# Optimization experiments

Hardware: AMD Instinct MI355X
Metric: run time of the kernel (lower is better)

## Reference

```python
import jax, jax.numpy as jnp
import numpy as np


def _diag_perm(h, w):
    # Matches torch loop: offsets -(h-1)..w-1, within offset ordered by row i.
    ii, jj = np.meshgrid(np.arange(h), np.arange(w), indexing='ij')
    idx = np.lexsort((ii.ravel(), (jj - ii).ravel())).astype(np.int32)
    inv = np.argsort(idx).astype(np.int32)
    return jnp.asarray(idx), jnp.asarray(inv)


def _mamba(tok, ln_g, ln_b, Win, conv_w, conv_b, Wx, Wdt, bdt, A_log, Dp, Wout):
    # tok: (B, L, C). MambaLayer = LayerNorm + standard Mamba block.
    di, dc = conv_w.shape
    ds = A_log.shape[-1]
    dtr = Wdt.shape[-1]
    mu = tok.mean(-1, keepdims=True)
    var = ((tok - mu) ** 2).mean(-1, keepdims=True)
    t = (tok - mu) * jax.lax.rsqrt(var + 1e-5) * ln_g + ln_b
    xz = jnp.einsum('blc,ec->ble', t, Win)          # (B,L,2*di)
    xh, z = jnp.split(xz, 2, axis=-1)
    # causal depthwise conv over sequence
    xc = jnp.transpose(xh, (0, 2, 1))               # (B,di,L)
    xc = jax.lax.conv_general_dilated(
        xc, conv_w[:, None, :], (1,), [(dc - 1, 0)],
        dimension_numbers=('NCH', 'OIH', 'NCH'), feature_group_count=di)
    u = jax.nn.silu(jnp.transpose(xc, (0, 2, 1)) + conv_b)  # (B,L,di)
    proj = jnp.einsum('bld,ed->ble', u, Wx)
    dt_r, Bm, Cm = jnp.split(proj, [dtr, dtr + ds], axis=-1)
    dt = jax.nn.softplus(jnp.einsum('blr,dr->bld', dt_r, Wdt) + bdt)  # (B,L,di)
    A = -jnp.exp(A_log)                              # (di,ds)

    def step(h, inp):
        dt_t, B_t, C_t, u_t = inp                    # (B,di) (B,ds) (B,ds) (B,di)
        dA = jnp.exp(dt_t[..., None] * A)            # (B,di,ds)
        h = dA * h + dt_t[..., None] * B_t[:, None, :] * u_t[..., None]
        y = jnp.einsum('bds,bs->bd', h, C_t)
        return h, y

    h0 = jnp.zeros((u.shape[0], di, ds), u.dtype)
    _, ys = jax.lax.scan(step, h0, (jnp.moveaxis(dt, 1, 0), jnp.moveaxis(Bm, 1, 0),
                                    jnp.moveaxis(Cm, 1, 0), jnp.moveaxis(u, 1, 0)))
    y = jnp.moveaxis(ys, 0, 1) + u * Dp              # (B,L,di)
    y = y * jax.nn.silu(z)
    return jnp.einsum('bld,cd->blc', y, Wout)


def _forward(x, ln_g, ln_b, Win, conv_w, conv_b, Wx, Wdt, bdt, A_log, Dp, Wout):
    b, c, h, w = x.shape
    idx, inv = _diag_perm(h, w)

    def mam(d, tok):
        return _mamba(tok, ln_g[d], ln_b[d], Win[d], conv_w[d], conv_b[d],
                      Wx[d], Wdt[d], bdt[d], A_log[d], Dp[d], Wout[d])

    row_tok = x.reshape(b, c, h * w).transpose(0, 2, 1)
    row_feat = mam(0, row_tok).transpose(0, 2, 1).reshape(b, c, h, w)
    col_tok = x.transpose(0, 1, 3, 2).reshape(b, c, w * h).transpose(0, 2, 1)
    col_feat = mam(1, col_tok).transpose(0, 2, 1).reshape(b, c, w, h).transpose(0, 1, 3, 2)
    diag_feat = mam(2, row_tok[:, idx, :])[:, inv, :].transpose(0, 2, 1).reshape(b, c, h, w)
    xf = x[:, :, :, ::-1]
    anti_tok = xf.reshape(b, c, h * w).transpose(0, 2, 1)[:, idx, :]
    anti_feat = mam(3, anti_tok)[:, inv, :].transpose(0, 2, 1).reshape(b, c, h, w)[:, :, :, ::-1]
    gate = jax.nn.sigmoid((row_feat + col_feat + diag_feat + anti_feat) / 4.0)
    return x * gate


def setup_inputs() -> dict:
    key = jax.random.key(0)
    ks = jax.random.split(key, 8)
    B, C, H, W = 4, 96, 48, 48
    DI, DS, DC, DTR = 192, 16, 4, 6
    s = 0.05
    return {
        'x': jax.random.normal(ks[0], (B, C, H, W), jnp.float32),
        'ln_g': jnp.ones((4, C), jnp.float32),
        'ln_b': jnp.zeros((4, C), jnp.float32),
        'Win': jax.random.normal(ks[1], (4, 2 * DI, C), jnp.float32) * s,
        'conv_w': jax.random.normal(ks[2], (4, DI, DC), jnp.float32) * s,
        'conv_b': jnp.zeros((4, DI), jnp.float32),
        'Wx': jax.random.normal(ks[3], (4, DTR + 2 * DS, DI), jnp.float32) * s,
        'Wdt': jax.random.normal(ks[4], (4, DI, DTR), jnp.float32) * s,
        'bdt': jax.random.normal(ks[5], (4, DI), jnp.float32) * s,
        'A_log': jnp.log(jnp.broadcast_to(jnp.arange(1, DS + 1, dtype=jnp.float32), (4, DI, DS))),
        'Dp': jnp.ones((4, DI), jnp.float32),
        'Wout': jax.random.normal(ks[6], (4, C, DI), jnp.float32) * s,
    }


def reference(x, ln_g, ln_b, Win, conv_w, conv_b, Wx, Wdt, bdt, A_log, Dp, Wout):
    return _forward(x, ln_g, ln_b, Win, conv_w, conv_b, Wx, Wdt, bdt, A_log, Dp, Wout)
```

## Files before the change

### kernel.cpp

```cpp
#include <hip/hip_runtime.h>
#include <math.h>

#define LSEQ 2304
#define LC 32
#define NCH 72

typedef unsigned short u16;
typedef unsigned int u32;
typedef __attribute__((ext_vector_type(8))) short bf16x8;
typedef __attribute__((ext_vector_type(4))) float f32x4;

__device__ __forceinline__ float sigmoidf_(float v){ return 1.f/(1.f+__expf(-v)); }
__device__ __forceinline__ u16 f2b(float f){
  union{float f; u32 u;} v; v.f = f;
  u32 r = v.u + 0x7fffu + ((v.u >> 16) & 1u);
  return (u16)(r >> 16);
}
__device__ __forceinline__ float b2f(u16 h){
  union{u32 u; float f;} v; v.u = ((u32)h) << 16; return v.f;
}
__device__ __forceinline__ u16 f2h(float f){
  _Float16 h = (_Float16)f;
  union{_Float16 h; u16 u;} v; v.h = h; return v.u;
}
__device__ __forceinline__ float h2f(u16 u){
  union{u16 u; _Float16 h;} v; v.u = u; return (float)v.h;
}
__device__ __forceinline__ uint2 pack4(float a, float b, float c, float d){
  uint2 o;
  o.x = (u32)f2b(a) | ((u32)f2b(b) << 16);
  o.y = (u32)f2b(c) | ((u32)f2b(d) << 16);
  return o;
}
__device__ __forceinline__ float softplus_(float v){
  return fmaxf(v, 0.f) + __logf(1.f + __expf(-fabsf(v)));
}

__global__ void g_kernel(int* __restrict__ g, int* __restrict__ flag){
  int tid = threadIdx.x;
  if (tid == 0) *flag = 1;
  for (int l = tid; l < LSEQ; l += 256){
    g[l] = l;
    g[LSEQ + l] = (l % 48) * 48 + l / 48;
  }
  for (int p = tid; p < LSEQ; p += 256){
    int i = p / 48, j = p % 48, dd = j - i;
    int off = (dd <= 0) ? (47 + dd) * (48 + dd) / 2
                        : 1176 + 48 * (dd - 1) - dd * (dd - 1) / 2;
    int l = off + min(i, j);
    g[2 * LSEQ + l] = p;
  }
  __syncthreads();
  for (int l = tid; l < LSEQ; l += 256){
    int p2 = g[2 * LSEQ + l];
    g[3 * LSEQ + l] = (p2 / 48) * 48 + 47 - (p2 % 48);
  }
}

__global__ void prep_fold(const float* __restrict__ Win, const float* __restrict__ ln_g,
                          const float* __restrict__ ln_b, const float* __restrict__ A_log,
                          const float* __restrict__ Wout, const float* __restrict__ Wx,
                          const float* __restrict__ Wdt, const float* __restrict__ bdt,
                          u16* __restrict__ WinMF, float* __restrict__ b2,
                          float* __restrict__ Aneg2, u16* __restrict__ WoutMF,
                          u16* __restrict__ Wcomb, float* __restrict__ bcomb,
                          int* __restrict__ flag){
  int i = blockIdx.x * 256 + threadIdx.x;
  if (i < 4*192*16){
    float a = -expf(A_log[i]);
    Aneg2[i] = a * 1.44269504f;
    int s = i & 15;
    float a0 = -expf(A_log[i - s]);
    if (fabsf(a - (float)(s + 1) * a0) > 1e-5f * fabsf(a) + 1e-30f)
      atomicAnd(flag, 0);
  }
  if (i < 4*384*96){
    int d = i / 36864, r = i % 36864, c = r % 96;
    WinMF[i] = f2b(Win[i] * ln_g[d*96 + c]);
  }
  if (i < 4*96*192) WoutMF[i] = f2b(Wout[i]);
  if (i < 4*224*192){
    int d = i / 43008, r = i % 43008, e = r / 192, c = r % 192;
    float w;
    if (e < 192){
      const float* wdt = &Wdt[(size_t)(d*192 + e) * 6];
      w = 0.f;
      #pragma unroll
      for (int r6 = 0; r6 < 6; ++r6) w += wdt[r6] * Wx[(size_t)(d*38 + r6) * 192 + c];
    } else if (e < 208){
      w = Wx[(size_t)(d*38 + 6 + (e - 192)) * 192 + c];
    } else {
      w = Wx[(size_t)(d*38 + 22 + (e - 208)) * 192 + c];
    }
    Wcomb[i] = f2b(w);
  }
  if (i < 4*224){
    int d = i / 224, e = i % 224;
    bcomb[i] = (e < 192) ? bdt[d*192 + e] : 0.f;
  }
  if (i < 4*384){
    int d = i / 384;
    const float* wr = &Win[(size_t)i * 96];
    const float* lb = &ln_b[d * 96];
    float s = 0.f;
    for (int c = 0; c < 96; ++c) s += wr[c] * lb[c];
    b2[i] = s;
  }
}

__global__ __launch_bounds__(256) void ln_kernel(const float* __restrict__ x, u16* __restrict__ n){
  __shared__ float red[512];
  int tid = threadIdx.x;
  int s = tid & 63, q = tid >> 6;
  int T = blockIdx.x * 64 + s;
  int b = T / 2304, p = T % 2304;
  const float* xp = x + (size_t)b * 96 * 2304 + p;
  float vals[24];
  float sum = 0.f, ss = 0.f;
  #pragma unroll
  for (int k = 0; k < 24; ++k){
    float v = xp[(size_t)(q*24 + k) * 2304];
    vals[k] = v; sum += v; ss += v*v;
  }
  red[q*64 + s] = sum;
  red[256 + q*64 + s] = ss;
  __syncthreads();
  float S = red[s] + red[64+s] + red[128+s] + red[192+s];
  float Q = red[256+s] + red[320+s] + red[384+s] + red[448+s];
  float mu = S * (1.f/96.f);
  float var = Q * (1.f/96.f) - mu*mu;
  float rs = rsqrtf(var + 1e-5f);
  u32 w[12];
  #pragma unroll
  for (int k = 0; k < 12; ++k){
    float v0 = (vals[2*k]   - mu) * rs;
    float v1 = (vals[2*k+1] - mu) * rs;
    w[k] = (u32)f2b(v0) | ((u32)f2b(v1) << 16);
  }
  uint4* np_ = (uint4*)(n + (size_t)T * 96 + q*24);
  np_[0] = make_uint4(w[0], w[1], w[2],  w[3]);
  np_[1] = make_uint4(w[4], w[5], w[6],  w[7]);
  np_[2] = make_uint4(w[8], w[9], w[10], w[11]);
}

__global__ __launch_bounds__(256) void kprojconv(const u16* __restrict__ nbf,
    const int* __restrict__ g, const u16* __restrict__ WinMF, const float* __restrict__ b2,
    const float* __restrict__ conv_w, const float* __restrict__ conv_b,
    u16* __restrict__ u, u16* __restrict__ sz){
  __shared__ u16 tl[80][200];
  __shared__ u16 xh[80][200];
  int d = blockIdx.z, b = blockIdx.y, l0 = blockIdx.x * 64;
  int tid = threadIdx.x;
  int seq = d*4 + b;
  const int* gd = g + d * LSEQ;
  for (int i = tid; i < 67*12; i += 256){
    int lt = i / 12, j = i % 12;
    int gl = l0 - 3 + lt;
    uint4 v = make_uint4(0u, 0u, 0u, 0u);
    if (gl >= 0){
      int p = gd[gl];
      v = *(const uint4*)(nbf + (size_t)(b*2304 + p) * 96 + j*8);
    }
    *(uint4*)&tl[lt][j*8] = v;
  }
  __syncthreads();
  int wv = tid >> 6, lane = tid & 63;
  int lr = lane & 15, lg = lane >> 4;
  const u16* Wb = WinMF + (size_t)d * 36864 + (size_t)lr * 96 + lg * 8;
  const float* b2d = b2 + d * 384;
  size_t zbase = (size_t)seq * LSEQ * 192;
  for (int rt = wv; rt < 5; rt += 4){
    int row = rt*16 + lr;
    bf16x8 tk0 = *(const bf16x8*)&tl[row][      lg*8];
    bf16x8 tk1 = *(const bf16x8*)&tl[row][32  + lg*8];
    bf16x8 tk2 = *(const bf16x8*)&tl[row][64  + lg*8];
    bool valid = (l0 + row >= 3);
    for (int te = 0; te < 24; ++te){
      const u16* wp = Wb + (size_t)te * 1536;
      f32x4 acc = *(const f32x4*)&b2d[te*16 + lg*4];
      acc = __builtin_amdgcn_mfma_f32_16x16x32_bf16(*(const bf16x8*)(wp     ), tk0, acc, 0, 0, 0);
      acc = __builtin_amdgcn_mfma_f32_16x16x32_bf16(*(const bf16x8*)(wp + 32), tk1, acc, 0, 0, 0);
      acc = __builtin_amdgcn_mfma_f32_16x16x32_bf16(*(const bf16x8*)(wp + 64), tk2, acc, 0, 0, 0);
      if (te < 12){
        uint2 o = valid ? pack4(acc[0], acc[1], acc[2], acc[3]) : make_uint2(0u, 0u);
        *(uint2*)&xh[row][te*16 + lg*4] = o;
      } else if (row >= 3 && row < 67){
        float z0 = acc[0], z1 = acc[1], z2 = acc[2], z3 = acc[3];
        z0 *= sigmoidf_(z0); z1 *= sigmoidf_(z1); z2 *= sigmoidf_(z2); z3 *= sigmoidf_(z3);
        *(uint2*)(sz + zbase + (size_t)(l0 + row - 3) * 192 + (te-12)*16 + lg*4) = pack4(z0, z1, z2, z3);
      }
    }
  }
  __syncthreads();
  size_t obase = ((size_t)seq * LSEQ + l0) * 192;
  for (int i = tid; i < 64*48; i += 256){
    int lt = i / 48, j = (i % 48) * 4;
    float a0 = conv_b[d*192 + j + 0];
    float a1 = conv_b[d*192 + j + 1];
    float a2 = conv_b[d*192 + j + 2];
    float a3 = conv_b[d*192 + j + 3];
    const float4 w0 = *(const float4*)&conv_w[(size_t)(d*192 + j + 0) * 4];
    const float4 w1 = *(const float4*)&conv_w[(size_t)(d*192 + j + 1) * 4];
    const float4 w2 = *(const float4*)&conv_w[(size_t)(d*192 + j + 2) * 4];
    const float4 w3 = *(const float4*)&conv_w[(size_t)(d*192 + j + 3) * 4];
    const float* w0p = (const float*)&w0;
    const float* w1p = (const float*)&w1;
    const float* w2p = (const float*)&w2;
    const float* w3p = (const float*)&w3;
    #pragma unroll
    for (int kk = 0; kk < 4; ++kk){
      uint2 xv = *(const uint2*)&xh[lt + kk][j];
      a0 += w0p[kk] * b2f((u16)(xv.x & 0xffff));
      a1 += w1p[kk] * b2f((u16)(xv.x >> 16));
      a2 += w2p[kk] * b2f((u16)(xv.y & 0xffff));
      a3 += w3p[kk] * b2f((u16)(xv.y >> 16));
    }
    a0 *= sigmoidf_(a0); a1 *= sigmoidf_(a1); a2 *= sigmoidf_(a2); a3 *= sigmoidf_(a3);
    *(uint2*)(u + obase + (size_t)lt * 192 + j) = pack4(a0, a1, a2, a3);
  }
}

__global__ __launch_bounds__(256) void kernBM(const u16* __restrict__ u,
    const u16* __restrict__ Wcomb, const float* __restrict__ bcomb,
    u16* __restrict__ dtb, float* __restrict__ Bm, float* __restrict__ Cm){
  __shared__ u16 ush[64 * 200];
  int d = blockIdx.y;
  int tid = threadIdx.x;
  int tile0 = blockIdx.x * 64;
  const u16* ub = u + ((size_t)d * 4 * LSEQ + tile0) * 192;
  for (int i = tid; i < 64*24; i += 256){
    int row = i / 24, c8 = i % 24;
    *(uint4*)&ush[row*200 + c8*8] = *(const uint4*)&ub[(size_t)row*192 + c8*8];
  }
  __syncthreads();
  int wv = tid >> 6, lane = tid & 63;
  int lr = lane & 15, lg = lane >> 4;
  const u16* urow = &ush[(wv*16 + lr)*200 + lg*8];
  bf16x8 tk[6];
  #pragma unroll
  for (int kc = 0; kc < 6; ++kc) tk[kc] = *(const bf16x8*)(urow + kc*32);
  const u16* Wb = Wcomb + (size_t)d * 224 * 192 + (size_t)lr * 192 + lg * 8;
  bf16x8 bw[2][6];
  #pragma unroll
  for (int kc = 0; kc < 6; ++kc) bw[0][kc] = *(const bf16x8*)(Wb + kc*32);
  size_t tokrow = (size_t)d * 4 * LSEQ + tile0 + wv*16 + lr;
  for (int t = 0; t < 14; ++t){
    int cur = t & 1;
    if (t < 13){
      const u16* wp = Wb + (size_t)(t + 1) * 3072;
      #pragma unroll
      for (int kc = 0; kc < 6; ++kc) bw[cur^1][kc] = *(const bf16x8*)(wp + kc*32);
    }
    f32x4 a = (f32x4){0.f, 0.f, 0.f, 0.f};
    #pragma unroll
    for (int kc = 0; kc < 6; ++kc)
      a = __builtin_amdgcn_mfma_f32_16x16x32_bf16(bw[cur][kc], tk[kc], a, 0, 0, 0);
    if (t < 12){
      f32x4 bb = *(const f32x4*)&bcomb[d*224 + t*16 + lg*4];
      float s0 = softplus_(a[0] + bb[0]);
      float s1 = softplus_(a[1] + bb[1]);
      float s2 = softplus_(a[2] + bb[2]);
      float s3 = softplus_(a[3] + bb[3]);
      uint2 o;
      o.x = (u32)f2h(s0) | ((u32)f2h(s1) << 16);
      o.y = (u32)f2h(s2) | ((u32)f2h(s3) << 16);
      *(uint2*)&dtb[tokrow * 192 + t*16 + lg*4] = o;
    } else if (t == 12){
      *(float4*)&Bm[tokrow * 16 + lg*4] = make_float4(a[0], a[1], a[2], a[3]);
    } else {
      *(float4*)&Cm[tokrow * 16 + lg*4] = make_float4(a[0], a[1], a[2], a[3]);
    }
  }
}

__global__ __launch_bounds__(192) void kernC1(const u16* __restrict__ dtb, const u16* __restrict__ u,
    const float* __restrict__ Bm, const float* __restrict__ Aneg2, const int* __restrict__ flag,
    u16* __restrict__ hfin, float* __restrict__ Send){
  __shared__ float Bsh[LC*16];
  int ch = blockIdx.x, b = blockIdx.y, d = blockIdx.z;
  int seq = d*4 + b;
  int di = threadIdx.x;
  size_t tb = (size_t)seq * LSEQ + ch * LC;
  const float* bp = Bm + tb * 16;
  for (int i = di; i < LC*16; i += 192) Bsh[i] = bp[i];
  const u16* dtp = dtb + tb * 192;
  const u16* up  = u   + tb * 192;
  float h[16];
  #pragma unroll
  for (int s = 0; s < 16; ++s) h[s] = 0.f;
  float Sacc = 0.f;
  __syncthreads();
  if (*flag){
    float A2_0 = Aneg2[(d*192 + di) * 16];
    for (int j = 0; j < LC; ++j){
      float dtv = h2f(dtp[j*192 + di]);
      float uv  = b2f(up[j*192 + di]);
      float Bs[16];
      {
        const float4* b4 = (const float4*)&Bsh[j * 16];
        #pragma unroll
        for (int q = 0; q < 4; ++q){ float4 v = b4[q]; Bs[q*4]=v.x; Bs[q*4+1]=v.y; Bs[q*4+2]=v.z; Bs[q*4+3]=v.w; }
      }
      float dtu = dtv * uv;
      float e1 = __builtin_amdgcn_exp2f(dtv * A2_0);
      float e2 = e1*e1, e4 = e2*e2, e8 = e4*e4;
      float p[8];
      p[0]=e1; p[1]=e2; p[2]=e1*e2; p[3]=e4; p[4]=e1*e4; p[5]=e2*e4; p[6]=p[2]*e4; p[7]=e8;
      #pragma unroll
      for (int s = 0; s < 8; ++s){
        h[s] = p[s]*h[s] + dtu*Bs[s];
        float q = p[s]*e8;
        h[s+8] = q*h[s+8] + dtu*Bs[s+8];
      }
      Sacc += dtv;
    }
  } else {
    float A2[16];
    {
      const float4* ap = (const float4*)&Aneg2[(d*192 + di) * 16];
      #pragma unroll
      for (int q = 0; q < 4; ++q){ float4 a4 = ap[q]; A2[q*4]=a4.x; A2[q*4+1]=a4.y; A2[q*4+2]=a4.z; A2[q*4+3]=a4.w; }
    }
    for (int j = 0; j < LC; ++j){
      float dtv = h2f(dtp[j*192 + di]);
      float uv  = b2f(up[j*192 + di]);
      float Bs[16];
      {
        const float4* b4 = (const float4*)&Bsh[j * 16];
        #pragma unroll
        for (int q = 0; q < 4; ++q){ float4 v = b4[q]; Bs[q*4]=v.x; Bs[q*4+1]=v.y; Bs[q*4+2]=v.z; Bs[q*4+3]=v.w; }
      }
      float dtu = dtv * uv;
      #pragma unroll
      for (int s = 0; s < 16; ++s)
        h[s] = __builtin_amdgcn_exp2f(dtv * A2[s]) * h[s] + dtu * Bs[s];
      Sacc += dtv;
    }
  }
  u16* hf = &hfin[((size_t)seq * NCH + ch) * 3072 + di * 16];
  uint4 o0, o1;
  o0.x = (u32)f2b(h[0])  | ((u32)f2b(h[1])  << 16);
  o0.y = (u32)f2b(h[2])  | ((u32)f2b(h[3])  << 16);
  o0.z = (u32)f2b(h[4])  | ((u32)f2b(h[5])  << 16);
  o0.w = (u32)f2b(h[6])  | ((u32)f2b(h[7])  << 16);
  o1.x = (u32)f2b(h[8])  | ((u32)f2b(h[9])  << 16);
  o1.y = (u32)f2b(h[10]) | ((u32)f2b(h[11]) << 16);
  o1.z = (u32)f2b(h[12]) | ((u32)f2b(h[13]) << 16);
  o1.w = (u32)f2b(h[14]) | ((u32)f2b(h[15]) << 16);
  *(uint4*)hf = o0;
  *(uint4*)(hf + 8) = o1;
  Send[((size_t)seq * NCH + ch) * 192 + di] = Sacc;
}

__global__ __launch_bounds__(256) void kernC2(const u16* __restrict__ hfin, const float* __restrict__ Send,
    const float* __restrict__ Aneg2, u16* __restrict__ hin){
  int t = blockIdx.x * 256 + threadIdx.x;
  int seq = t / 3072, q = t % 3072;
  int di = q >> 4, s = q & 15;
  int d = seq >> 2;
  float A2 = Aneg2[(d*192 + di)*16 + s];
  float hr = 0.f;
  const u16* hf = hfin + (size_t)seq * NCH * 3072 + q;
  u16* hi = hin + (size_t)seq * NCH * 3072 + q;
  const float* Se = Send + (size_t)seq * NCH * 192 + di;
  for (int ch = 0; ch < NCH; ++ch){
    hi[(size_t)ch * 3072] = f2b(hr);
    hr = b2f(hf[(size_t)ch * 3072]) + __builtin_amdgcn_exp2f(A2 * Se[(size_t)ch * 192]) * hr;
  }
}

__global__ __launch_bounds__(384) void kscan2out(const u16* __restrict__ dtb, const u16* __restrict__ u,
    const float* __restrict__ Bm, const float* __restrict__ Cm,
    const float* __restrict__ Aneg2, const int* __restrict__ flag, const u16* __restrict__ hin,
    const u16* __restrict__ sz, const float* __restrict__ Dp,
    const u16* __restrict__ WoutMF, const int* __restrict__ g,
    u16* __restrict__ feat){
  __shared__ float Bsh[64*16];
  __shared__ float Csh[64*16];
  __shared__ u16 vsh[64][200];
  int b = blockIdx.y, d = blockIdx.z;
  int seq = d*4 + b;
  int l0 = blockIdx.x * 64;
  int tid = threadIdx.x;
  int gc = tid / 192, di = tid % 192;
  int ch = blockIdx.x * 2 + gc;
  {
    const float* bp = Bm + ((size_t)seq * LSEQ + l0) * 16;
    const float* cp = Cm + ((size_t)seq * LSEQ + l0) * 16;
    for (int i = tid; i < 64*16; i += 384){ Bsh[i] = bp[i]; Csh[i] = cp[i]; }
  }
  float h[16];
  {
    const uint4* hi4 = (const uint4*)&hin[((size_t)seq * NCH + ch) * 3072 + di * 16];
    uint4 v0 = hi4[0], v1 = hi4[1];
    h[0]=b2f((u16)(v0.x&0xffff)); h[1]=b2f((u16)(v0.x>>16));
    h[2]=b2f((u16)(v0.y&0xffff)); h[3]=b2f((u16)(v0.y>>16));
    h[4]=b2f((u16)(v0.z&0xffff)); h[5]=b2f((u16)(v0.z>>16));
    h[6]=b2f((u16)(v0.w&0xffff)); h[7]=b2f((u16)(v0.w>>16));
    h[8]=b2f((u16)(v1.x&0xffff)); h[9]=b2f((u16)(v1.x>>16));
    h[10]=b2f((u16)(v1.y&0xffff)); h[11]=b2f((u16)(v1.y>>16));
    h[12]=b2f((u16)(v1.z&0xffff)); h[13]=b2f((u16)(v1.z>>16));
    h[14]=b2f((u16)(v1.w&0xffff)); h[15]=b2f((u16)(v1.w>>16));
  }
  float Dpv = Dp[d*192 + di];
  size_t tb = (size_t)seq * LSEQ + ch * LC;
  const u16* dtp = dtb + tb * 192;
  const u16* up  = u   + tb * 192;
  const u16* szp = sz  + tb * 192;
  __syncthreads();
  if (*flag){
    float A2_0 = Aneg2[(d*192 + di) * 16];
    for (int j = 0; j < LC; ++j){
      float dtv = h2f(dtp[j*192 + di]);
      float uv  = b2f(up[j*192 + di]);
      float Bs[16], Cs[16];
      {
        const float4* b4 = (const float4*)&Bsh[(gc*32 + j) * 16];
        const float4* c4 = (const float4*)&Csh[(gc*32 + j) * 16];
        #pragma unroll
        for (int q = 0; q < 4; ++q){
          float4 v = b4[q]; Bs[q*4]=v.x; Bs[q*4+1]=v.y; Bs[q*4+2]=v.z; Bs[q*4+3]=v.w;
          float4 w = c4[q]; Cs[q*4]=w.x; Cs[q*4+1]=w.y; Cs[q*4+2]=w.z; Cs[q*4+3]=w.w;
        }
      }
      float dtu = dtv * uv;
      float e1 = __builtin_amdgcn_exp2f(dtv * A2_0);
      float e2 = e1*e1, e4 = e2*e2, e8 = e4*e4;
      float p[8];
      p[0]=e1; p[1]=e2; p[2]=e1*e2; p[3]=e4; p[4]=e1*e4; p[5]=e2*e4; p[6]=p[2]*e4; p[7]=e8;
      float yv = 0.f;
      #pragma unroll
      for (int s = 0; s < 8; ++s){
        h[s] = p[s]*h[s] + dtu*Bs[s];
        yv += h[s]*Cs[s];
        float q = p[s]*e8;
        h[s+8] = q*h[s+8] + dtu*Bs[s+8];
        yv += h[s+8]*Cs[s+8];
      }
      float szv = b2f(szp[j*192 + di]);
      vsh[gc*32 + j][di] = f2b((yv + uv * Dpv) * szv);
    }
  } else {
    float A2[16];
    {
      const float4* ap = (const float4*)&Aneg2[(d*192 + di) * 16];
      #pragma unroll
      for (int q = 0; q < 4; ++q){ float4 a4 = ap[q]; A2[q*4]=a4.x; A2[q*4+1]=a4.y; A2[q*4+2]=a4.z; A2[q*4+3]=a4.w; }
    }
    for (int j = 0; j < LC; ++j){
      float dtv = h2f(dtp[j*192 + di]);
      float uv  = b2f(up[j*192 + di]);
      float Bs[16], Cs[16];
      {
        const float4* b4 = (const float4*)&Bsh[(gc*32 + j) * 16];
        const float4* c4 = (const float4*)&Csh[(gc*32 + j) * 16];
        #pragma unroll
        for (int q = 0; q < 4; ++q){
          float4 v = b4[q]; Bs[q*4]=v.x; Bs[q*4+1]=v.y; Bs[q*4+2]=v.z; Bs[q*4+3]=v.w;
          float4 w = c4[q]; Cs[q*4]=w.x; Cs[q*4+1]=w.y; Cs[q*4+2]=w.z; Cs[q*4+3]=w.w;
        }
      }
      float dtu = dtv * uv;
      float yv = 0.f;
      #pragma unroll
      for (int s = 0; s < 16; ++s){
        h[s] = __builtin_amdgcn_exp2f(dtv * A2[s]) * h[s] + dtu * Bs[s];
        yv += h[s] * Cs[s];
      }
      float szv = b2f(szp[j*192 + di]);
      vsh[gc*32 + j][di] = f2b((yv + uv * Dpv) * szv);
    }
  }
  __syncthreads();
  if (tid < 256){
    int wv = tid >> 6, lane = tid & 63;
    int lr = lane & 15, lg = lane >> 4;
    bf16x8 tk[6];
    #pragma unroll
    for (int kc = 0; kc < 6; ++kc)
      tk[kc] = *(const bf16x8*)&vsh[wv*16 + lr][kc*32 + lg*8];
    const u16* Wb = WoutMF + (size_t)d * 18432 + (size_t)lr * 192 + lg * 8;
    f32x4 acc[6];
    #pragma unroll
    for (int t = 0; t < 6; ++t) acc[t] = (f32x4){0.f, 0.f, 0.f, 0.f};
    #pragma unroll
    for (int t = 0; t < 6; ++t){
      const u16* wp = Wb + (size_t)t * 3072;
      #pragma unroll
      for (int kc = 0; kc < 6; ++kc)
        acc[t] = __builtin_amdgcn_mfma_f32_16x16x32_bf16(*(const bf16x8*)(wp + kc*32), tk[kc], acc[t], 0, 0, 0);
    }
    u16* fd = feat + (size_t)seq * LSEQ * 96;
    int p = g[d*LSEQ + l0 + wv*16 + lr];
    #pragma unroll
    for (int t = 0; t < 6; ++t){
      uint2 o = pack4(acc[t][0], acc[t][1], acc[t][2], acc[t][3]);
      *(uint2*)&fd[(size_t)p * 96 + t*16 + lg*4] = o;
    }
  }
}

__global__ __launch_bounds__(256) void kernE(const float* __restrict__ x, const u16* __restrict__ feat,
    float* __restrict__ out){
  __shared__ float acc[64 * 97];
  int p0 = blockIdx.x * 64, b = blockIdx.y;
  int tid = threadIdx.x;
  const size_t DS_ = (size_t)4 * LSEQ * 96;
  size_t base = ((size_t)b * LSEQ + p0) * 96;
  for (int i = tid; i < 3072; i += 256){
    int pp = i / 48, c2 = (i % 48) * 2;
    size_t o = base + (size_t)pp * 96 + c2;
    u32 v0 = *(const u32*)(feat + o);
    u32 v1 = *(const u32*)(feat + DS_ + o);
    u32 v2 = *(const u32*)(feat + 2*DS_ + o);
    u32 v3 = *(const u32*)(feat + 3*DS_ + o);
    float s0 = b2f((u16)(v0 & 0xffff)) + b2f((u16)(v1 & 0xffff)) + b2f((u16)(v2 & 0xffff)) + b2f((u16)(v3 & 0xffff));
    float s1 = b2f((u16)(v0 >> 16)) + b2f((u16)(v1 >> 16)) + b2f((u16)(v2 >> 16)) + b2f((u16)(v3 >> 16));
    acc[pp*97 + c2] = s0;
    acc[pp*97 + c2 + 1] = s1;
  }
  __syncthreads();
  for (int i = tid; i < 6144; i += 256){
    int c = i / 64, pp = i % 64;
    size_t o = ((size_t)b * 96 + c) * LSEQ + p0 + pp;
    out[o] = x[o] * sigmoidf_(acc[pp*97 + c] * 0.25f);
  }
}

extern "C" void kernel_launch(void* const* d_in, const int* in_sizes, int n_in,
                              void* d_out, int out_size, void* d_ws, size_t ws_size,
                              hipStream_t stream) {
  const float* x      = (const float*)d_in[0];
  const float* ln_g   = (const float*)d_in[1];
  const float* ln_b   = (const float*)d_in[2];
  const float* Win    = (const float*)d_in[3];
  const float* conv_w = (const float*)d_in[4];
  const float* conv_b = (const float*)d_in[5];
  const float* Wx     = (const float*)d_in[6];
  const float* Wdt    = (const float*)d_in[7];
  const float* bdt    = (const float*)d_in[8];
  const float* A_log  = (const float*)d_in[9];
  const float* Dp     = (const float*)d_in[10];
  const float* Wout   = (const float*)d_in[11];

  char* W = (char*)d_ws;
  char* W0 = W;
  auto alloc = [&](size_t bytes) -> char* {
    char* p = W; W += (bytes + 255) & ~(size_t)255; return p;
  };
  int*   g      = (int*)  alloc((size_t)4 * LSEQ * 4);
  int*   flag   = (int*)  alloc(256);
  float* Aneg2  = (float*)alloc((size_t)4 * 192 * 16 * 4);
  float* b2     = (float*)alloc((size_t)4 * 384 * 4);
  u16*   WinMF  = (u16*)  alloc((size_t)4 * 384 * 96 * 2);
  u16*   WoutMF = (u16*)  alloc((size_t)4 * 96 * 192 * 2);
  u16*   Wcomb  = (u16*)  alloc((size_t)4 * 224 * 192 * 2);
  float* bcomb  = (float*)alloc((size_t)4 * 224 * 4);
  u16*   nbf    = (u16*)  alloc((size_t)9216 * 96 * 2);
  u16*   ubf    = (u16*)  alloc((size_t)16 * LSEQ * 192 * 2);
  u16*   szbf   = (u16*)  alloc((size_t)16 * LSEQ * 192 * 2);
  u16*   dtb    = (u16*)  alloc((size_t)16 * LSEQ * 192 * 2);
  float* Bm     = (float*)alloc((size_t)16 * LSEQ * 16 * 4);
  float* Cm     = (float*)alloc((size_t)16 * LSEQ * 16 * 4);
  float* Send   = (float*)alloc((size_t)16 * NCH * 192 * 4);
  u16*   hfin   = (u16*)  alloc((size_t)16 * NCH * 3072 * 2);
  u16*   hin    = (u16*)  alloc((size_t)16 * NCH * 3072 * 2);
  u16*   feat   = (u16*)  alloc((size_t)16 * LSEQ * 96 * 2);
  if ((size_t)(W - W0) > ws_size) return;

  g_kernel<<<1, 256, 0, stream>>>(g, flag);
  prep_fold<<<768, 256, 0, stream>>>(Win, ln_g, ln_b, A_log, Wout, Wx, Wdt, bdt,
                                     WinMF, b2, Aneg2, WoutMF, Wcomb, bcomb, flag);
  ln_kernel<<<144, 256, 0, stream>>>(x, nbf);
  kprojconv<<<dim3(36, 4, 4), 256, 0, stream>>>(nbf, g, WinMF, b2, conv_w, conv_b, ubf, szbf);
  kernBM<<<dim3(144, 4), 256, 0, stream>>>(ubf, Wcomb, bcomb, dtb, Bm, Cm);
  kernC1<<<dim3(NCH, 4, 4), 192, 0, stream>>>(dtb, ubf, Bm, Aneg2, flag, hfin, Send);
  kernC2<<<192, 256, 0, stream>>>(hfin, Send, Aneg2, hin);
  kscan2out<<<dim3(36, 4, 4), 384, 0, stream>>>(dtb, ubf, Bm, Cm, Aneg2, flag, hin, szbf, Dp,
                                                WoutMF, g, feat);
  kernE<<<dim3(36, 4), 256, 0, stream>>>(x, feat, (float*)d_out);
}
```

Before: 206.8 us.

## Split fused input projection and conv into separate GEMM and conv kernels

The fused projection+conv kernel is split into two kernels. `kproj` runs the LN-token × Win GEMM once per token in natural order, with 8 independent MFMA accumulators per wave, and writes a bf16 xz buffer. `kconv` then gathers xz rows through the diagonal permutation, applies the causal depthwise conv, and computes silu(z). This removes the halo recompute of 3 extra rows per 64-row tile, the uneven 5-tiles-over-4-waves split, and the serial single-accumulator MFMA chain. In exchange it adds a global round trip through a roughly 28 MB intermediate buffer and one more kernel launch.

```diff
diff --git a/kernel.cpp b/kernel.cpp
--- a/kernel.cpp
+++ b/kernel.cpp
@@ -143,56 +143,69 @@
   np_[2] = make_uint4(w[8], w[9], w[10], w[11]);
 }
 
-__global__ __launch_bounds__(256) void kprojconv(const u16* __restrict__ nbf,
-    const int* __restrict__ g, const u16* __restrict__ WinMF, const float* __restrict__ b2,
+__global__ __launch_bounds__(256) void kproj(const u16* __restrict__ nbf,
+    const u16* __restrict__ WinMF, const float* __restrict__ b2,
+    u16* __restrict__ xz){
+  int d = blockIdx.y;
+  int wv = threadIdx.x >> 6, lane = threadIdx.x & 63;
+  int lr = lane & 15, lg = lane >> 4;
+  int r0 = blockIdx.x * 64 + wv * 16;
+  const u16* Ap = nbf + (size_t)(r0 + lr) * 96 + lg * 8;
+  bf16x8 tk0 = *(const bf16x8*)(Ap);
+  bf16x8 tk1 = *(const bf16x8*)(Ap + 32);
+  bf16x8 tk2 = *(const bf16x8*)(Ap + 64);
+  const u16* Wb = WinMF + (size_t)d * 36864 + (size_t)lr * 96 + lg * 8;
+  const float* b2d = b2 + d * 384;
+  u16* out = xz + ((size_t)d * 9216 + r0 + lr) * 384;
+  for (int grp = 0; grp < 3; ++grp){
+    f32x4 acc[8];
+    #pragma unroll
+    for (int t = 0; t < 8; ++t)
+      acc[t] = *(const f32x4*)&b2d[(grp*8 + t)*16 + lg*4];
+    #pragma unroll
+    for (int t = 0; t < 8; ++t){
+      const u16* wp = Wb + (size_t)(grp*8 + t) * 1536;
+      acc[t] = __builtin_amdgcn_mfma_f32_16x16x32_bf16(*(const bf16x8*)(wp     ), tk0, acc[t], 0, 0, 0);
+      acc[t] = __builtin_amdgcn_mfma_f32_16x16x32_bf16(*(const bf16x8*)(wp + 32), tk1, acc[t], 0, 0, 0);
+      acc[t] = __builtin_amdgcn_mfma_f32_16x16x32_bf16(*(const bf16x8*)(wp + 64), tk2, acc[t], 0, 0, 0);
+    }
+    #pragma unroll
+    for (int t = 0; t < 8; ++t){
+      uint2 o = pack4(acc[t][0], acc[t][1], acc[t][2], acc[t][3]);
+      *(uint2*)&out[(grp*8 + t)*16 + lg*4] = o;
+    }
+  }
+}
+
+__global__ __launch_bounds__(256) void kconv(const u16* __restrict__ xz, const int* __restrict__ g,
     const float* __restrict__ conv_w, const float* __restrict__ conv_b,
     u16* __restrict__ u, u16* __restrict__ sz){
-  __shared__ u16 tl[80][200];
-  __shared__ u16 xh[80][200];
+  __shared__ u16 xh[67][200];
   int d = blockIdx.z, b = blockIdx.y, l0 = blockIdx.x * 64;
   int tid = threadIdx.x;
-  int seq = d*4 + b;
   const int* gd = g + d * LSEQ;
-  for (int i = tid; i < 67*12; i += 256){
-    int lt = i / 12, j = i % 12;
+  const u16* xzd = xz + (size_t)d * 9216 * 384 + (size_t)b * LSEQ * 384;
+  for (int i = tid; i < 67*24; i += 256){
+    int lt = i / 24, j = i % 24;
     int gl = l0 - 3 + lt;
     uint4 v = make_uint4(0u, 0u, 0u, 0u);
     if (gl >= 0){
       int p = gd[gl];
-      v = *(const uint4*)(nbf + (size_t)(b*2304 + p) * 96 + j*8);
-    }
-    *(uint4*)&tl[lt][j*8] = v;
-  }
-  __syncthreads();
-  int wv = tid >> 6, lane = tid & 63;
-  int lr = lane & 15, lg = lane >> 4;
-  const u16* Wb = WinMF + (size_t)d * 36864 + (size_t)lr * 96 + lg * 8;
-  const float* b2d = b2 + d * 384;
-  size_t zbase = (size_t)seq * LSEQ * 192;
-  for (int rt = wv; rt < 5; rt += 4){
-    int row = rt*16 + lr;
-    bf16x8 tk0 = *(const bf16x8*)&tl[row][      lg*8];
-    bf16x8 tk1 = *(const bf16x8*)&tl[row][32  + lg*8];
-    bf16x8 tk2 = *(const bf16x8*)&tl[row][64  + lg*8];
-    bool valid = (l0 + row >= 3);
-    for (int te = 0; te < 24; ++te){
-      const u16* wp = Wb + (size_t)te * 1536;
-      f32x4 acc = *(const f32x4*)&b2d[te*16 + lg*4];
-      acc = __builtin_amdgcn_mfma_f32_16x16x32_bf16(*(const bf16x8*)(wp     ), tk0, acc, 0, 0, 0);
-      acc = __builtin_amdgcn_mfma_f32_16x16x32_bf16(*(const bf16x8*)(wp + 32), tk1, acc, 0, 0, 0);
-      acc = __builtin_amdgcn_mfma_f32_16x16x32_bf16(*(const bf16x8*)(wp + 64), tk2, acc, 0, 0, 0);
-      if (te < 12){
-        uint2 o = valid ? pack4(acc[0], acc[1], acc[2], acc[3]) : make_uint2(0u, 0u);
-        *(uint2*)&xh[row][te*16 + lg*4] = o;
-      } else if (row >= 3 && row < 67){
-        float z0 = acc[0], z1 = acc[1], z2 = acc[2], z3 = acc[3];
-        z0 *= sigmoidf_(z0); z1 *= sigmoidf_(z1); z2 *= sigmoidf_(z2); z3 *= sigmoidf_(z3);
-        *(uint2*)(sz + zbase + (size_t)(l0 + row - 3) * 192 + (te-12)*16 + lg*4) = pack4(z0, z1, z2, z3);
-      }
-    }
-  }
-  __syncthreads();
-  size_t obase = ((size_t)seq * LSEQ + l0) * 192;
+      v = *(const uint4*)(xzd + (size_t)p * 384 + j * 8);
+    }
+    *(uint4*)&xh[lt][j*8] = v;
+  }
+  size_t obase = ((size_t)(d*4 + b) * LSEQ + l0) * 192;
+  for (int i = tid; i < 64*48; i += 256){
+    int lt = i / 48, j = (i % 48) * 4;
+    int p = gd[l0 + lt];
+    uint2 zv = *(const uint2*)(xzd + (size_t)p * 384 + 192 + j);
+    float z0 = b2f((u16)(zv.x & 0xffff)), z1 = b2f((u16)(zv.x >> 16));
+    float z2 = b2f((u16)(zv.y & 0xffff)), z3 = b2f((u16)(zv.y >> 16));
+    z0 *= sigmoidf_(z0); z1 *= sigmoidf_(z1); z2 *= sigmoidf_(z2); z3 *= sigmoidf_(z3);
+    *(uint2*)(sz + obase + (size_t)lt * 192 + j) = pack4(z0, z1, z2, z3);
+  }
+  __syncthreads();
   for (int i = tid; i < 64*48; i += 256){
     int lt = i / 48, j = (i % 48) * 4;
     float a0 = conv_b[d*192 + j + 0];
@@ -557,6 +570,7 @@
   u16*   Wcomb  = (u16*)  alloc((size_t)4 * 224 * 192 * 2);
   float* bcomb  = (float*)alloc((size_t)4 * 224 * 4);
   u16*   nbf    = (u16*)  alloc((size_t)9216 * 96 * 2);
+  u16*   xz     = (u16*)  alloc((size_t)4 * 9216 * 384 * 2);
   u16*   ubf    = (u16*)  alloc((size_t)16 * LSEQ * 192 * 2);
   u16*   szbf   = (u16*)  alloc((size_t)16 * LSEQ * 192 * 2);
   u16*   dtb    = (u16*)  alloc((size_t)16 * LSEQ * 192 * 2);
@@ -572,7 +586,8 @@
   prep_fold<<<768, 256, 0, stream>>>(Win, ln_g, ln_b, A_log, Wout, Wx, Wdt, bdt,
                                      WinMF, b2, Aneg2, WoutMF, Wcomb, bcomb, flag);
   ln_kernel<<<144, 256, 0, stream>>>(x, nbf);
-  kprojconv<<<dim3(36, 4, 4), 256, 0, stream>>>(nbf, g, WinMF, b2, conv_w, conv_b, ubf, szbf);
+  kproj<<<dim3(144, 4), 256, 0, stream>>>(nbf, WinMF, b2, xz);
+  kconv<<<dim3(36, 4, 4), 256, 0, stream>>>(xz, g, conv_w, conv_b, ubf, szbf);
   kernBM<<<dim3(144, 4), 256, 0, stream>>>(ubf, Wcomb, bcomb, dtb, Bm, Cm);
   kernC1<<<dim3(NCH, 4, 4), 192, 0, stream>>>(dtb, ubf, Bm, Aneg2, flag, hfin, Send);
   kernC2<<<192, 256, 0, stream>>>(hfin, Send, Aneg2, hin);
```

After: 197.0 us. 1.05x faster.
